# Kernel optimization log

Measured on AMD Instinct MI355X. Metric: run time of the kernel, lower is better.

## Reference

```python
import jax, jax.numpy as jnp
import numpy as np

B, L, D_MODEL = 2, 4096, 512
HEADS = 8
DH = D_MODEL // HEADS
M = 266  # round(DH * ln(DH)) = round(64 * 4.1589)


def setup_inputs() -> dict:
    key = jax.random.key(0)
    ks = jax.random.split(key, 12)
    s = 0.02
    d = D_MODEL
    return {
        "query": jax.random.normal(ks[0], (B, L, d), jnp.float32),
        "key": jax.random.normal(ks[1], (B, L, d), jnp.float32),
        "value": jax.random.normal(ks[2], (B, L, d), jnp.float32),
        "Wq": jax.random.normal(ks[3], (d, d), jnp.float32) * s,
        "bq": jnp.zeros((d,), jnp.float32),
        "Wk": jax.random.normal(ks[4], (d, d), jnp.float32) * s,
        "bk": jnp.zeros((d,), jnp.float32),
        "Wv": jax.random.normal(ks[5], (d, d), jnp.float32) * s,
        "bv": jnp.zeros((d,), jnp.float32),
        "Wout": jax.random.normal(ks[6], (d, d), jnp.float32) * s,
        "bout": jnp.zeros((d,), jnp.float32),
        "random_features": jax.random.normal(ks[7], (M, DH), jnp.float32),
    }


def reference(query, key, value, Wq, bq, Wk, bk, Wv, bv, Wout, bout, random_features):
    bs, sl, dm = query.shape
    H, Dh = HEADS, dm // HEADS

    def lin(x, W, b):
        return x @ W.T + b

    def to_heads(x):  # [B,L,dm] -> [L,B,H,Dh]  (matches torch [L,B,H,*] layout)
        return x.reshape(bs, sl, H, Dh).transpose(1, 0, 2, 3)

    q = to_heads(lin(query, Wq, bq))
    k = to_heads(lin(key, Wk, bk))
    v = to_heads(lin(value, Wv, bv))

    scale = dm ** 0.25
    q = q / scale
    k = k / scale

    # project onto random features: W_t is random_features^T, [Dh,M]
    pq = jnp.einsum('lbhd,md->lbhm', q, random_features)
    pk = jnp.einsum('lbhd,md->lbhm', k, random_features)
    # exp kernel: exp(h + x) with h = -||x||^2 / 2
    hq = -0.5 * jnp.sum(q * q, axis=-1, keepdims=True)
    hk = -0.5 * jnp.sum(k * k, axis=-1, keepdims=True)
    q_prime = jnp.exp(hq + pq)  # [L,B,H,M]
    k_prime = jnp.exp(hk + pk)  # [L,B,H,M]

    # Causal FAVOR+ numerator/denominator via prefix-sum recurrence (lax.scan over L)
    def step(carry, xs):
        S, z = carry           # S: [B,H,M,Dh], z: [B,H,M]
        qt, kt, vt = xs        # [B,H,M], [B,H,M], [B,H,Dh]
        S = S + kt[..., None] * vt[..., None, :]
        z = z + kt
        num = jnp.einsum('bhmd,bhm->bhd', S, qt)
        den = jnp.einsum('bhm,bhm->bh', qt, z)
        return (S, z), (num, den)

    S0 = jnp.zeros((bs, H, M, Dh), q.dtype)
    z0 = jnp.zeros((bs, H, M), q.dtype)
    _, (num, den) = jax.lax.scan(step, (S0, z0), (q_prime, k_prime, v))

    attn = num / den[..., None]                     # [L,B,H,Dh]
    ctx = attn.transpose(1, 0, 2, 3).reshape(bs, sl, dm)
    return ctx @ Wout.T + bout
```

## Files before the change

kernel.cpp:

```cpp
#include <hip/hip_runtime.h>
#include <hip/hip_bf16.h>

#define L_ 4096
#define MP 272
#define BH16 16

typedef __attribute__((ext_vector_type(8))) __bf16 bf16x8;
typedef __attribute__((ext_vector_type(4))) float f32x4;

__device__ inline __bf16 f2b(float f) {
    unsigned u = __float_as_uint(f);
    unsigned r = (u + 0x7fffu + ((u >> 16) & 1u)) >> 16;
    unsigned short s = (unsigned short)r;
    return *reinterpret_cast<__bf16*>(&s);
}
__device__ inline float b2f(__bf16 b) {
    unsigned short s = *reinterpret_cast<unsigned short*>(&b);
    return __uint_as_float(((unsigned)s) << 16);
}

#define NW 262144
__global__ __launch_bounds__(256) void prep2(
    const float* __restrict__ Wq, const float* __restrict__ Wk, const float* __restrict__ Wv,
    const float* __restrict__ Wout, const float* __restrict__ RF,
    __bf16* __restrict__ Wqb, __bf16* __restrict__ Wkb, __bf16* __restrict__ Wvb,
    __bf16* __restrict__ Woutb, __bf16* __restrict__ RFb, __bf16* __restrict__ vT)
{
    long idx = (long)blockIdx.x * 256 + threadIdx.x;
    if (idx < NW) { Wqb[idx] = f2b(Wq[idx]); return; }  idx -= NW;
    if (idx < NW) { Wkb[idx] = f2b(Wk[idx]); return; }  idx -= NW;
    if (idx < NW) { Wvb[idx] = f2b(Wv[idx]); return; }  idx -= NW;
    if (idx < NW) { Woutb[idx] = f2b(Wout[idx]); return; }  idx -= NW;
    if (idx < MP * 64) { int row = (int)(idx >> 6); RFb[idx] = f2b(row < 266 ? RF[idx] : 0.f); return; }
    idx -= MP * 64;
    if (idx < 65536) {
        int bh = (int)(idx >> 12), l = (int)(idx & 4095);
        vT[((size_t)bh * 65 + 64) * L_ + l] = f2b(1.f);
    }
}

template<int AF32, int EPI>
__global__ __launch_bounds__(512) void proj(
    const void* __restrict__ Ap, const __bf16* __restrict__ W,
    const float* __restrict__ bias, void* __restrict__ O,
    float* __restrict__ hout, float scale)
{
    __shared__ __bf16 Al[128 * 40];
    __shared__ __bf16 Bl[64 * 40];
    const int t = threadIdx.x;
    const int w = t >> 6, lane = t & 63;
    const int m0 = blockIdx.x * 128, n0 = blockIdx.y * 64;

    f32x4 acc[4];
    #pragma unroll
    for (int j = 0; j < 4; ++j) acc[j] = f32x4{0.f,0.f,0.f,0.f};

    float4 a_f[2];
    unsigned a_h[4];
    unsigned b_r[2];

    auto LOADT = [&](int ks) {
        const int kk = ks * 32;
        if constexpr (AF32) {
            const float* A = (const float*)Ap;
            #pragma unroll
            for (int it = 0; it < 2; ++it) {
                int u = t + it * 512; int r = u >> 3, q4 = (u & 7) << 2;
                a_f[it] = *(const float4*)&A[(size_t)(m0 + r) * 512 + kk + q4];
            }
        } else {
            const __bf16* A = (const __bf16*)Ap;
            #pragma unroll
            for (int it = 0; it < 4; ++it) {
                int u = t + it * 512; int r = u >> 4, dw = (u & 15) << 1;
                a_h[it] = *(const unsigned*)&A[(size_t)(m0 + r) * 512 + kk + dw];
            }
        }
        #pragma unroll
        for (int it = 0; it < 2; ++it) {
            int u = t + it * 512; int r = u >> 4, dw = (u & 15) << 1;
            b_r[it] = *(const unsigned*)&W[(size_t)(n0 + r) * 512 + kk + dw];
        }
    };
    auto STORET = [&]() {
        if constexpr (AF32) {
            #pragma unroll
            for (int it = 0; it < 2; ++it) {
                int u = t + it * 512; int r = u >> 3, q4 = (u & 7) << 2;
                __bf16* d = &Al[r * 40 + q4];
                d[0] = f2b(a_f[it].x); d[1] = f2b(a_f[it].y);
                d[2] = f2b(a_f[it].z); d[3] = f2b(a_f[it].w);
            }
        } else {
            #pragma unroll
            for (int it = 0; it < 4; ++it) {
                int u = t + it * 512; int r = u >> 4, dw = (u & 15) << 1;
                *(unsigned*)&Al[r * 40 + dw] = a_h[it];
            }
        }
        #pragma unroll
        for (int it = 0; it < 2; ++it) {
            int u = t + it * 512; int r = u >> 4, dw = (u & 15) << 1;
            *(unsigned*)&Bl[r * 40 + dw] = b_r[it];
        }
    };

    LOADT(0);
    for (int ks = 0; ks < 16; ++ks) {
        __syncthreads();
        STORET();
        __syncthreads();
        if (ks < 15) LOADT(ks + 1);
        bf16x8 af = *(const bf16x8*)&Al[(w * 16 + (lane & 15)) * 40 + (lane >> 4) * 8];
        #pragma unroll
        for (int j = 0; j < 4; ++j) {
            bf16x8 bf = *(const bf16x8*)&Bl[(j * 16 + (lane & 15)) * 40 + (lane >> 4) * 8];
            acc[j] = __builtin_amdgcn_mfma_f32_16x16x32_bf16(af, bf, acc[j], 0, 0, 0);
        }
    }

    if constexpr (EPI == 1) {
        __shared__ __bf16 Tv[64 * 136];
        #pragma unroll
        for (int j = 0; j < 4; ++j)
            #pragma unroll
            for (int e = 0; e < 4; ++e) {
                int rl = w * 16 + ((lane >> 4) << 2) + e;
                int cn = n0 + j * 16 + (lane & 15);
                Tv[(cn & 63) * 136 + rl] = f2b(acc[j][e] + bias[cn]);
            }
        __syncthreads();
        __bf16* vT = (__bf16*)O;
        int b = m0 >> 12, l0 = m0 & 4095, h = n0 >> 6;
        #pragma unroll
        for (int it = 0; it < 2; ++it) {
            int v = t + it * 512;
            int d = v >> 4, seg = v & 15;
            *(uint4*)&vT[((size_t)(b * 8 + h) * 65 + d) * L_ + l0 + seg * 8] =
                *(const uint4*)&Tv[d * 136 + seg * 8];
        }
    } else if constexpr (EPI == 0) {
        float sred[4] = {0.f, 0.f, 0.f, 0.f};
        #pragma unroll
        for (int j = 0; j < 4; ++j)
            #pragma unroll
            for (int e = 0; e < 4; ++e) {
                int r = m0 + w * 16 + ((lane >> 4) << 2) + e;
                int cn = n0 + j * 16 + (lane & 15);
                float vv = (acc[j][e] + bias[cn]) * scale;
                int b = r >> 12, l = r & 4095, h = cn >> 6, d = cn & 63;
                ((__bf16*)O)[(((size_t)(b * 8 + h) * L_ + l) << 6) + d] = f2b(vv);
                sred[e] += vv * vv;
            }
        #pragma unroll
        for (int e = 0; e < 4; ++e) {
            float s = sred[e];
            s += __shfl_xor(s, 1); s += __shfl_xor(s, 2);
            s += __shfl_xor(s, 4); s += __shfl_xor(s, 8);
            if ((lane & 15) == 0) {
                int r = m0 + w * 16 + ((lane >> 4) << 2) + e;
                int bh = (r >> 12) * 8 + (n0 >> 6);
                hout[(size_t)bh * 4096 + (r & 4095)] = -0.5f * s;
            }
        }
    } else {
        #pragma unroll
        for (int j = 0; j < 4; ++j)
            #pragma unroll
            for (int e = 0; e < 4; ++e) {
                int r = m0 + w * 16 + ((lane >> 4) << 2) + e;
                int cn = n0 + j * 16 + (lane & 15);
                ((float*)O)[(size_t)r * 512 + cn] = acc[j][e] + bias[cn];
            }
    }
}

__global__ __launch_bounds__(256) void chunk_sums4(
    const __bf16* __restrict__ kh, const __bf16* __restrict__ vT,
    const float* __restrict__ hk, const __bf16* __restrict__ RFb,
    __bf16* __restrict__ ScT)
{
    __shared__ char arena[41472];
    __bf16* RFl = (__bf16*)(arena);
    __bf16* KPl = (__bf16*)(arena + 9216);
    __bf16* Vl  = (__bf16*)(arena + 18432);
    __bf16* T2  = (__bf16*)(arena + 29952);
    const int t = threadIdx.x;
    const int w = t >> 6, lane = t & 63;
    const int z = blockIdx.x, zb = z & 15, zc = z >> 4;
    const __bf16* kh_b = kh + (size_t)zb * 262144 + (size_t)(zc * 64) * 64;
    const __bf16* vT_b = vT + (size_t)zb * 266240 + (size_t)zc * 64;
    __bf16* Obase = ScT + (size_t)(zc * 16 + zb) * 17680;

    bf16x8 ak[2];
    #pragma unroll
    for (int ks = 0; ks < 2; ++ks)
        ak[ks] = *(const bf16x8*)&kh_b[(size_t)(w * 16 + (lane & 15)) * 64 + ks * 32 + (lane >> 4) * 8];
    float hkr[4];
    #pragma unroll
    for (int e = 0; e < 4; ++e)
        hkr[e] = hk[(size_t)zb * 4096 + zc * 64 + w * 16 + ((lane >> 4) << 2) + e];

    #pragma unroll
    for (int it = 0; it < 9; ++it) {
        int u = t + it * 256;
        if (u < 2080) {
            int d = u >> 5, lp = (u & 31) << 1;
            *(unsigned*)&Vl[d * 72 + lp] = *(const unsigned*)&vT_b[(size_t)d * L_ + lp];
        }
    }

    for (int mt = 0; mt < 5; ++mt) {
        const int m0 = mt * 64;
        __syncthreads();
        #pragma unroll
        for (int it = 0; it < 8; ++it) {
            int u = t + it * 256; int r = u >> 5, lp = (u & 31) << 1;
            unsigned v = (m0 + r < MP) ? *(const unsigned*)&RFb[(size_t)(m0 + r) * 64 + lp] : 0u;
            *(unsigned*)&RFl[r * 72 + lp] = v;
        }
        __syncthreads();
        f32x4 acck[4];
        #pragma unroll
        for (int j = 0; j < 4; ++j) acck[j] = f32x4{0.f,0.f,0.f,0.f};
        #pragma unroll
        for (int ks = 0; ks < 2; ++ks)
            #pragma unroll
            for (int j = 0; j < 4; ++j) {
                bf16x8 bf = *(const bf16x8*)&RFl[(j * 16 + (lane & 15)) * 72 + ks * 32 + (lane >> 4) * 8];
                acck[j] = __builtin_amdgcn_mfma_f32_16x16x32_bf16(ak[ks], bf, acck[j], 0, 0, 0);
            }
        #pragma unroll
        for (int j = 0; j < 4; ++j)
            #pragma unroll
            for (int e = 0; e < 4; ++e) {
                int rl = w * 16 + ((lane >> 4) << 2) + e;
                int cn = j * 16 + (lane & 15);
                float v = (m0 + cn < 266) ? __expf(hkr[e] + acck[j][e]) : 0.f;
                KPl[cn * 72 + rl] = f2b(v);
            }
        __syncthreads();
        f32x4 accS[5];
        #pragma unroll
        for (int j = 0; j < 5; ++j) accS[j] = f32x4{0.f,0.f,0.f,0.f};
        #pragma unroll
        for (int ks = 0; ks < 2; ++ks) {
            bf16x8 af = *(const bf16x8*)&KPl[(w * 16 + (lane & 15)) * 72 + ks * 32 + (lane >> 4) * 8];
            #pragma unroll
            for (int j = 0; j < 5; ++j) {
                bf16x8 bf = *(const bf16x8*)&Vl[(j * 16 + (lane & 15)) * 72 + ks * 32 + (lane >> 4) * 8];
                accS[j] = __builtin_amdgcn_mfma_f32_16x16x32_bf16(af, bf, accS[j], 0, 0, 0);
            }
        }
        #pragma unroll
        for (int j = 0; j < 5; ++j)
            #pragma unroll
            for (int e = 0; e < 4; ++e) {
                int rl = w * 16 + ((lane >> 4) << 2) + e;
                int cn = j * 16 + (lane & 15);
                T2[cn * 72 + rl] = f2b(accS[j][e]);
            }
        __syncthreads();
        for (int v2 = t; v2 < 65 * 8; v2 += 256) {
            int row = v2 >> 3, seg = v2 & 7;
            if (m0 + seg * 8 < MP)
                *(uint4*)&Obase[(size_t)row * MP + m0 + seg * 8] = *(const uint4*)&T2[row * 72 + seg * 8];
        }
    }
}

__global__ __launch_bounds__(256) void prefixk(__bf16* __restrict__ ScT)
{
    int idx = blockIdx.x * 256 + threadIdx.x;
    const int STRIDE = BH16 * 65 * MP;
    if (idx >= STRIDE) return;
    __bf16* p = ScT + idx;
    float run = 0.f;
    #pragma unroll 1
    for (int cb = 0; cb < 8; ++cb) {
        float v[8];
        #pragma unroll
        for (int i = 0; i < 8; ++i) v[i] = b2f(p[(size_t)(cb * 8 + i) * STRIDE]);
        #pragma unroll
        for (int i = 0; i < 8; ++i) { p[(size_t)(cb * 8 + i) * STRIDE] = f2b(run); run += v[i]; }
    }
}

__global__ __launch_bounds__(256) void fusedD2(
    const __bf16* __restrict__ qh, const __bf16* __restrict__ kh,
    const float* __restrict__ hq, const float* __restrict__ hk,
    const __bf16* __restrict__ RFb, const __bf16* __restrict__ ScT,
    const __bf16* __restrict__ vT, __bf16* __restrict__ ctx)
{
    __shared__ char arena[41728];
    __bf16* RFl = (__bf16*)(arena);
    __bf16* Vl  = (__bf16*)(arena);
    __bf16* B2l = (__bf16*)(arena + 11520);
    __bf16* Aq  = (__bf16*)(arena + 23040);
    __bf16* Bk  = (__bf16*)(arena + 32256);
    __bf16* Sl  = (__bf16*)(arena + 32256);
    float* sden = (float*)(arena + 41472);
    const int t = threadIdx.x;
    const int w = t >> 6, lane = t & 63;
    const int z = blockIdx.x, zb = z & 15, zc = z >> 4;
    const __bf16* qh_b = qh + (size_t)zb * 262144 + (size_t)(zc * 64) * 64;
    const __bf16* kh_b = kh + (size_t)zb * 262144 + (size_t)(zc * 64) * 64;
    const __bf16* Sp_b = ScT + (size_t)(zc * 16 + zb) * 17680;
    const __bf16* vT_b = vT + (size_t)zb * 266240 + (size_t)zc * 64;

    bf16x8 aq[2], ak[2];
    #pragma unroll
    for (int ks = 0; ks < 2; ++ks) {
        size_t off = (size_t)(w * 16 + (lane & 15)) * 64 + ks * 32 + (lane >> 4) * 8;
        aq[ks] = *(const bf16x8*)&qh_b[off];
        ak[ks] = *(const bf16x8*)&kh_b[off];
    }
    float hqr[4], hkr[4];
    #pragma unroll
    for (int e = 0; e < 4; ++e) {
        int rl = w * 16 + ((lane >> 4) << 2) + e;
        hqr[e] = hq[(size_t)zb * 4096 + zc * 64 + rl];
        hkr[e] = hk[(size_t)zb * 4096 + zc * 64 + rl];
    }
    unsigned v_r[10];
    #pragma unroll
    for (int it = 0; it < 10; ++it) {
        int u = t + it * 256; int d = u >> 5, lp = (u & 31) << 1;
        v_r[it] = (d < 65) ? *(const unsigned*)&vT_b[(size_t)d * L_ + lp] : 0u;
    }

    f32x4 acc1[4], acc2[5];
    #pragma unroll
    for (int j = 0; j < 4; ++j) acc1[j] = f32x4{0.f,0.f,0.f,0.f};
    #pragma unroll
    for (int j = 0; j < 5; ++j) acc2[j] = f32x4{0.f,0.f,0.f,0.f};

    for (int mt = 0; mt < 5; ++mt) {
        const int m0 = mt * 64;
        __syncthreads();
        #pragma unroll
        for (int it = 0; it < 8; ++it) {
            int u = t + it * 256; int r = u >> 5, lp = (u & 31) << 1;
            unsigned v = (m0 + r < MP) ? *(const unsigned*)&RFb[(size_t)(m0 + r) * 64 + lp] : 0u;
            *(unsigned*)&RFl[r * 72 + lp] = v;
        }
        #pragma unroll
        for (int it = 0; it < 9; ++it) {
            int u = t + it * 256;
            if (u < 2080) {
                int r = u >> 5, lp = (u & 31) << 1;
                unsigned v = (m0 + lp < MP) ? *(const unsigned*)&Sp_b[(size_t)r * MP + m0 + lp] : 0u;
                *(unsigned*)&B2l[r * 72 + lp] = v;
            }
        }
        __syncthreads();
        f32x4 accq[4], acck[4];
        #pragma unroll
        for (int j = 0; j < 4; ++j) { accq[j] = f32x4{0.f,0.f,0.f,0.f}; acck[j] = f32x4{0.f,0.f,0.f,0.f}; }
        #pragma unroll
        for (int ks = 0; ks < 2; ++ks)
            #pragma unroll
            for (int j = 0; j < 4; ++j) {
                bf16x8 bf = *(const bf16x8*)&RFl[(j * 16 + (lane & 15)) * 72 + ks * 32 + (lane >> 4) * 8];
                accq[j] = __builtin_amdgcn_mfma_f32_16x16x32_bf16(aq[ks], bf, accq[j], 0, 0, 0);
                acck[j] = __builtin_amdgcn_mfma_f32_16x16x32_bf16(ak[ks], bf, acck[j], 0, 0, 0);
            }
        #pragma unroll
        for (int j = 0; j < 4; ++j)
            #pragma unroll
            for (int e = 0; e < 4; ++e) {
                int rl = w * 16 + ((lane >> 4) << 2) + e;
                int cn = j * 16 + (lane & 15);
                bool ok = (m0 + cn) < 266;
                Aq[rl * 72 + cn] = f2b(ok ? __expf(hqr[e] + accq[j][e]) : 0.f);
                Bk[rl * 72 + cn] = f2b(ok ? __expf(hkr[e] + acck[j][e]) : 0.f);
            }
        __syncthreads();
        #pragma unroll
        for (int ks = 0; ks < 2; ++ks) {
            bf16x8 af = *(const bf16x8*)&Aq[(w * 16 + (lane & 15)) * 72 + ks * 32 + (lane >> 4) * 8];
            #pragma unroll
            for (int j = 0; j < 4; ++j) {
                bf16x8 bf = *(const bf16x8*)&Bk[(j * 16 + (lane & 15)) * 72 + ks * 32 + (lane >> 4) * 8];
                acc1[j] = __builtin_amdgcn_mfma_f32_16x16x32_bf16(af, bf, acc1[j], 0, 0, 0);
            }
            #pragma unroll
            for (int j = 0; j < 5; ++j) {
                bf16x8 bf = *(const bf16x8*)&B2l[(j * 16 + (lane & 15)) * 72 + ks * 32 + (lane >> 4) * 8];
                acc2[j] = __builtin_amdgcn_mfma_f32_16x16x32_bf16(af, bf, acc2[j], 0, 0, 0);
            }
        }
    }
    __syncthreads();
    #pragma unroll
    for (int it = 0; it < 10; ++it) {
        int u = t + it * 256; int d = u >> 5, lp = (u & 31) << 1;
        *(unsigned*)&Vl[d * 72 + lp] = v_r[it];
    }
    #pragma unroll
    for (int j = 0; j < 4; ++j)
        #pragma unroll
        for (int e = 0; e < 4; ++e) {
            int rl = w * 16 + ((lane >> 4) << 2) + e;
            int cn = j * 16 + (lane & 15);
            Sl[rl * 72 + cn] = f2b(rl >= cn ? acc1[j][e] : 0.f);
        }
    __syncthreads();
    #pragma unroll
    for (int ks2 = 0; ks2 < 2; ++ks2) {
        bf16x8 as = *(const bf16x8*)&Sl[(w * 16 + (lane & 15)) * 72 + ks2 * 32 + (lane >> 4) * 8];
        #pragma unroll
        for (int j = 0; j < 5; ++j) {
            bf16x8 bf = *(const bf16x8*)&Vl[(j * 16 + (lane & 15)) * 72 + ks2 * 32 + (lane >> 4) * 8];
            acc2[j] = __builtin_amdgcn_mfma_f32_16x16x32_bf16(as, bf, acc2[j], 0, 0, 0);
        }
    }
    if ((lane & 15) == 0) {
        #pragma unroll
        for (int e = 0; e < 4; ++e)
            sden[w * 16 + ((lane >> 4) << 2) + e] = acc2[4][e];
    }
    __syncthreads();
    const int b = zb >> 3, h = zb & 7;
    #pragma unroll
    for (int j = 0; j < 4; ++j)
        #pragma unroll
        for (int e = 0; e < 4; ++e) {
            int rl = w * 16 + ((lane >> 4) << 2) + e;
            int cn = j * 16 + (lane & 15);
            float val = acc2[j][e] / sden[rl];
            ctx[((size_t)(b * L_ + zc * 64 + rl)) * 512 + h * 64 + cn] = f2b(val);
        }
}

extern "C" void kernel_launch(void* const* d_in, const int* in_sizes, int n_in,
                              void* d_out, int out_size, void* d_ws, size_t ws_size,
                              hipStream_t stream) {
    const float* query = (const float*)d_in[0];
    const float* key   = (const float*)d_in[1];
    const float* value = (const float*)d_in[2];
    const float* Wq    = (const float*)d_in[3];
    const float* bq    = (const float*)d_in[4];
    const float* Wk    = (const float*)d_in[5];
    const float* bk    = (const float*)d_in[6];
    const float* Wv    = (const float*)d_in[7];
    const float* bv    = (const float*)d_in[8];
    const float* Wout  = (const float*)d_in[9];
    const float* bout  = (const float*)d_in[10];
    const float* RF    = (const float*)d_in[11];

    char* w8 = (char*)d_ws;
    __bf16* ctx  = (__bf16*)(w8 + 0);
    __bf16* qh   = (__bf16*)(w8 + 8388608);
    __bf16* kh   = (__bf16*)(w8 + 16777216);
    __bf16* vT   = (__bf16*)(w8 + 25165824);
    __bf16* ScT  = (__bf16*)(w8 + 33688576);
    __bf16* Wqb  = (__bf16*)(w8 + 69897216);
    __bf16* Wkb  = (__bf16*)(w8 + 70421504);
    __bf16* Wvb  = (__bf16*)(w8 + 70945792);
    __bf16* Woutb= (__bf16*)(w8 + 71470080);
    __bf16* RFb  = (__bf16*)(w8 + 71994368);
    float*  hq   = (float*) (w8 + 72029184);
    float*  hk   = (float*) (w8 + 72291328);

    const float qscale = 0.21022410381342865f;

    prep2<<<4420, 256, 0, stream>>>(Wq, Wk, Wv, Wout, RF, Wqb, Wkb, Wvb, Woutb, RFb, vT);

    dim3 gg(64, 8);
    proj<1,0><<<gg, 512, 0, stream>>>(query, Wqb, bq, qh, hq, qscale);
    proj<1,0><<<gg, 512, 0, stream>>>(key,   Wkb, bk, kh, hk, qscale);
    proj<1,1><<<gg, 512, 0, stream>>>(value, Wvb, bv, vT, nullptr, 1.f);

    chunk_sums4<<<1024, 256, 0, stream>>>(kh, vT, hk, RFb, ScT);

    prefixk<<<1105, 256, 0, stream>>>(ScT);

    fusedD2<<<1024, 256, 0, stream>>>(qh, kh, hq, hk, RFb, ScT, vT, ctx);

    proj<0,2><<<gg, 512, 0, stream>>>(ctx, Woutb, bout, d_out, nullptr, 1.f);
}
```

Baseline: 276.2 us.

## Register-prefetch next RF/prefix tiles and drop intra-tile barriers in FAVOR kernels

In both the chunk-sum kernel and the fused output kernel, the next m-tile of random features (and, in the fused kernel, the prefix-state tile) is loaded into registers while the current tile is computed. It is written to LDS at the end of the iteration, which leaves one barrier per tile instead of two. The chunk-sum kernel also swaps MFMA operand roles so that each wave owns the feature rows it writes, which removes the barrier between the exp step and the S accumulation. The fused kernel issues the Aq×S MFMAs before the barrier, because those rows are wave-private. The cost is higher register pressure, which could reduce occupancy.

```diff
diff --git a/kernel.cpp b/kernel.cpp
--- a/kernel.cpp
+++ b/kernel.cpp
@@ -175,12 +175,12 @@
     }
 }
 
-__global__ __launch_bounds__(256) void chunk_sums4(
+__global__ __launch_bounds__(256) void chunk_sums6(
     const __bf16* __restrict__ kh, const __bf16* __restrict__ vT,
     const float* __restrict__ hk, const __bf16* __restrict__ RFb,
     __bf16* __restrict__ ScT)
 {
-    __shared__ char arena[41472];
+    __shared__ char arena[39456];
     __bf16* RFl = (__bf16*)(arena);
     __bf16* KPl = (__bf16*)(arena + 9216);
     __bf16* Vl  = (__bf16*)(arena + 18432);
@@ -192,54 +192,66 @@
     const __bf16* vT_b = vT + (size_t)zb * 266240 + (size_t)zc * 64;
     __bf16* Obase = ScT + (size_t)(zc * 16 + zb) * 17680;
 
-    bf16x8 ak[2];
-    #pragma unroll
-    for (int ks = 0; ks < 2; ++ks)
-        ak[ks] = *(const bf16x8*)&kh_b[(size_t)(w * 16 + (lane & 15)) * 64 + ks * 32 + (lane >> 4) * 8];
-    float hkr[4];
-    #pragma unroll
-    for (int e = 0; e < 4; ++e)
-        hkr[e] = hk[(size_t)zb * 4096 + zc * 64 + w * 16 + ((lane >> 4) << 2) + e];
-
-    #pragma unroll
-    for (int it = 0; it < 9; ++it) {
-        int u = t + it * 256;
-        if (u < 2080) {
-            int d = u >> 5, lp = (u & 31) << 1;
-            *(unsigned*)&Vl[d * 72 + lp] = *(const unsigned*)&vT_b[(size_t)d * L_ + lp];
-        }
-    }
+    bf16x8 bkh[4][2];
+    #pragma unroll
+    for (int j = 0; j < 4; ++j)
+        #pragma unroll
+        for (int ks = 0; ks < 2; ++ks)
+            bkh[j][ks] = *(const bf16x8*)&kh_b[(size_t)(j * 16 + (lane & 15)) * 64 + ks * 32 + (lane >> 4) * 8];
+    float hk_c[4];
+    #pragma unroll
+    for (int j = 0; j < 4; ++j)
+        hk_c[j] = hk[(size_t)zb * 4096 + zc * 64 + j * 16 + (lane & 15)];
+
+    unsigned rf_r[8];
+    auto LOAD_RF = [&](int mt) {
+        const int m0 = mt * 64;
+        #pragma unroll
+        for (int it = 0; it < 8; ++it) {
+            int u = t + it * 256; int r = u >> 5, lp = (u & 31) << 1;
+            rf_r[it] = (m0 + r < MP) ? *(const unsigned*)&RFb[(size_t)(m0 + r) * 64 + lp] : 0u;
+        }
+    };
+    auto STAGE_RF = [&]() {
+        #pragma unroll
+        for (int it = 0; it < 8; ++it) {
+            int u = t + it * 256; int r = u >> 5, lp = (u & 31) << 1;
+            *(unsigned*)&RFl[r * 72 + lp] = rf_r[it];
+        }
+    };
+
+    #pragma unroll
+    for (int it = 0; it < 10; ++it) {
+        int u = t + it * 256; int d = u >> 5, lp = (u & 31) << 1;
+        unsigned v = (d < 65) ? *(const unsigned*)&vT_b[(size_t)d * L_ + lp] : 0u;
+        *(unsigned*)&Vl[d * 72 + lp] = v;
+    }
+    LOAD_RF(0);
+    STAGE_RF();
+    __syncthreads();
 
     for (int mt = 0; mt < 5; ++mt) {
         const int m0 = mt * 64;
-        __syncthreads();
-        #pragma unroll
-        for (int it = 0; it < 8; ++it) {
-            int u = t + it * 256; int r = u >> 5, lp = (u & 31) << 1;
-            unsigned v = (m0 + r < MP) ? *(const unsigned*)&RFb[(size_t)(m0 + r) * 64 + lp] : 0u;
-            *(unsigned*)&RFl[r * 72 + lp] = v;
-        }
-        __syncthreads();
+        if (mt < 4) LOAD_RF(mt + 1);
         f32x4 acck[4];
         #pragma unroll
         for (int j = 0; j < 4; ++j) acck[j] = f32x4{0.f,0.f,0.f,0.f};
         #pragma unroll
-        for (int ks = 0; ks < 2; ++ks)
-            #pragma unroll
-            for (int j = 0; j < 4; ++j) {
-                bf16x8 bf = *(const bf16x8*)&RFl[(j * 16 + (lane & 15)) * 72 + ks * 32 + (lane >> 4) * 8];
-                acck[j] = __builtin_amdgcn_mfma_f32_16x16x32_bf16(ak[ks], bf, acck[j], 0, 0, 0);
-            }
+        for (int ks = 0; ks < 2; ++ks) {
+            bf16x8 af = *(const bf16x8*)&RFl[(w * 16 + (lane & 15)) * 72 + ks * 32 + (lane >> 4) * 8];
+            #pragma unroll
+            for (int j = 0; j < 4; ++j)
+                acck[j] = __builtin_amdgcn_mfma_f32_16x16x32_bf16(af, bkh[j][ks], acck[j], 0, 0, 0);
+        }
         #pragma unroll
         for (int j = 0; j < 4; ++j)
             #pragma unroll
             for (int e = 0; e < 4; ++e) {
                 int rl = w * 16 + ((lane >> 4) << 2) + e;
                 int cn = j * 16 + (lane & 15);
-                float v = (m0 + cn < 266) ? __expf(hkr[e] + acck[j][e]) : 0.f;
-                KPl[cn * 72 + rl] = f2b(v);
-            }
-        __syncthreads();
+                float v = (m0 + rl < 266) ? __expf(hk_c[j] + acck[j][e]) : 0.f;
+                KPl[rl * 72 + cn] = f2b(v);
+            }
         f32x4 accS[5];
         #pragma unroll
         for (int j = 0; j < 5; ++j) accS[j] = f32x4{0.f,0.f,0.f,0.f};
@@ -258,7 +270,7 @@
             for (int e = 0; e < 4; ++e) {
                 int rl = w * 16 + ((lane >> 4) << 2) + e;
                 int cn = j * 16 + (lane & 15);
-                T2[cn * 72 + rl] = f2b(accS[j][e]);
+                if (cn < 66) T2[cn * 72 + rl] = f2b(accS[j][e]);
             }
         __syncthreads();
         for (int v2 = t; v2 < 65 * 8; v2 += 256) {
@@ -266,6 +278,8 @@
             if (m0 + seg * 8 < MP)
                 *(uint4*)&Obase[(size_t)row * MP + m0 + seg * 8] = *(const uint4*)&T2[row * 72 + seg * 8];
         }
+        if (mt < 4) STAGE_RF();
+        __syncthreads();
     }
 }
 
@@ -286,20 +300,20 @@
     }
 }
 
-__global__ __launch_bounds__(256) void fusedD2(
+__global__ __launch_bounds__(256) void fusedD3(
     const __bf16* __restrict__ qh, const __bf16* __restrict__ kh,
     const float* __restrict__ hq, const float* __restrict__ hk,
     const __bf16* __restrict__ RFb, const __bf16* __restrict__ ScT,
     const __bf16* __restrict__ vT, __bf16* __restrict__ ctx)
 {
-    __shared__ char arena[41728];
+    __shared__ char arena[39424];
     __bf16* RFl = (__bf16*)(arena);
+    __bf16* B2l = (__bf16*)(arena + 9216);
     __bf16* Vl  = (__bf16*)(arena);
-    __bf16* B2l = (__bf16*)(arena + 11520);
-    __bf16* Aq  = (__bf16*)(arena + 23040);
-    __bf16* Bk  = (__bf16*)(arena + 32256);
-    __bf16* Sl  = (__bf16*)(arena + 32256);
-    float* sden = (float*)(arena + 41472);
+    __bf16* Aq  = (__bf16*)(arena + 20736);
+    __bf16* Bk  = (__bf16*)(arena + 29952);
+    __bf16* Sl  = (__bf16*)(arena + 29952);
+    float* sden = (float*)(arena + 39168);
     const int t = threadIdx.x;
     const int w = t >> 6, lane = t & 63;
     const int z = blockIdx.x, zb = z & 15, zc = z >> 4;
@@ -308,12 +322,12 @@
     const __bf16* Sp_b = ScT + (size_t)(zc * 16 + zb) * 17680;
     const __bf16* vT_b = vT + (size_t)zb * 266240 + (size_t)zc * 64;
 
-    bf16x8 aq[2], ak[2];
+    bf16x8 aq[2], akk[2];
     #pragma unroll
     for (int ks = 0; ks < 2; ++ks) {
         size_t off = (size_t)(w * 16 + (lane & 15)) * 64 + ks * 32 + (lane >> 4) * 8;
         aq[ks] = *(const bf16x8*)&qh_b[off];
-        ak[ks] = *(const bf16x8*)&kh_b[off];
+        akk[ks] = *(const bf16x8*)&kh_b[off];
     }
     float hqr[4], hkr[4];
     #pragma unroll
@@ -329,31 +343,46 @@
         v_r[it] = (d < 65) ? *(const unsigned*)&vT_b[(size_t)d * L_ + lp] : 0u;
     }
 
+    unsigned rf_r[8], sp_r[10];
+    auto LOAD = [&](int mt) {
+        const int m0 = mt * 64;
+        #pragma unroll
+        for (int it = 0; it < 8; ++it) {
+            int u = t + it * 256; int r = u >> 5, lp = (u & 31) << 1;
+            rf_r[it] = (m0 + r < MP) ? *(const unsigned*)&RFb[(size_t)(m0 + r) * 64 + lp] : 0u;
+        }
+        #pragma unroll
+        for (int it = 0; it < 10; ++it) {
+            int u = t + it * 256; int r = u >> 5, lp = (u & 31) << 1;
+            sp_r[it] = (r < 65 && m0 + lp < MP) ? *(const unsigned*)&Sp_b[(size_t)r * MP + m0 + lp] : 0u;
+        }
+    };
+    auto STAGE = [&]() {
+        #pragma unroll
+        for (int it = 0; it < 8; ++it) {
+            int u = t + it * 256; int r = u >> 5, lp = (u & 31) << 1;
+            *(unsigned*)&RFl[r * 72 + lp] = rf_r[it];
+        }
+        #pragma unroll
+        for (int it = 0; it < 10; ++it) {
+            int u = t + it * 256; int r = u >> 5, lp = (u & 31) << 1;
+            *(unsigned*)&B2l[r * 72 + lp] = sp_r[it];
+        }
+    };
+
     f32x4 acc1[4], acc2[5];
     #pragma unroll
     for (int j = 0; j < 4; ++j) acc1[j] = f32x4{0.f,0.f,0.f,0.f};
     #pragma unroll
     for (int j = 0; j < 5; ++j) acc2[j] = f32x4{0.f,0.f,0.f,0.f};
+
+    LOAD(0);
+    STAGE();
+    __syncthreads();
 
     for (int mt = 0; mt < 5; ++mt) {
         const int m0 = mt * 64;
-        __syncthreads();
-        #pragma unroll
-        for (int it = 0; it < 8; ++it) {
-            int u = t + it * 256; int r = u >> 5, lp = (u & 31) << 1;
-            unsigned v = (m0 + r < MP) ? *(const unsigned*)&RFb[(size_t)(m0 + r) * 64 + lp] : 0u;
-            *(unsigned*)&RFl[r * 72 + lp] = v;
-        }
-        #pragma unroll
-        for (int it = 0; it < 9; ++it) {
-            int u = t + it * 256;
-            if (u < 2080) {
-                int r = u >> 5, lp = (u & 31) << 1;
-                unsigned v = (m0 + lp < MP) ? *(const unsigned*)&Sp_b[(size_t)r * MP + m0 + lp] : 0u;
-                *(unsigned*)&B2l[r * 72 + lp] = v;
-            }
-        }
-        __syncthreads();
+        if (mt < 4) LOAD(mt + 1);
         f32x4 accq[4], acck[4];
         #pragma unroll
         for (int j = 0; j < 4; ++j) { accq[j] = f32x4{0.f,0.f,0.f,0.f}; acck[j] = f32x4{0.f,0.f,0.f,0.f}; }
@@ -363,7 +392,7 @@
             for (int j = 0; j < 4; ++j) {
                 bf16x8 bf = *(const bf16x8*)&RFl[(j * 16 + (lane & 15)) * 72 + ks * 32 + (lane >> 4) * 8];
                 accq[j] = __builtin_amdgcn_mfma_f32_16x16x32_bf16(aq[ks], bf, accq[j], 0, 0, 0);
-                acck[j] = __builtin_amdgcn_mfma_f32_16x16x32_bf16(ak[ks], bf, acck[j], 0, 0, 0);
+                acck[j] = __builtin_amdgcn_mfma_f32_16x16x32_bf16(akk[ks], bf, acck[j], 0, 0, 0);
             }
         #pragma unroll
         for (int j = 0; j < 4; ++j)
@@ -375,23 +404,29 @@
                 Aq[rl * 72 + cn] = f2b(ok ? __expf(hqr[e] + accq[j][e]) : 0.f);
                 Bk[rl * 72 + cn] = f2b(ok ? __expf(hkr[e] + acck[j][e]) : 0.f);
             }
-        __syncthreads();
-        #pragma unroll
-        for (int ks = 0; ks < 2; ++ks) {
-            bf16x8 af = *(const bf16x8*)&Aq[(w * 16 + (lane & 15)) * 72 + ks * 32 + (lane >> 4) * 8];
+        bf16x8 af[2];
+        #pragma unroll
+        for (int ks = 0; ks < 2; ++ks)
+            af[ks] = *(const bf16x8*)&Aq[(w * 16 + (lane & 15)) * 72 + ks * 32 + (lane >> 4) * 8];
+        #pragma unroll
+        for (int ks = 0; ks < 2; ++ks)
+            #pragma unroll
+            for (int j = 0; j < 5; ++j) {
+                bf16x8 bf = *(const bf16x8*)&B2l[(j * 16 + (lane & 15)) * 72 + ks * 32 + (lane >> 4) * 8];
+                acc2[j] = __builtin_amdgcn_mfma_f32_16x16x32_bf16(af[ks], bf, acc2[j], 0, 0, 0);
+            }
+        __syncthreads();
+        #pragma unroll
+        for (int ks = 0; ks < 2; ++ks)
             #pragma unroll
             for (int j = 0; j < 4; ++j) {
                 bf16x8 bf = *(const bf16x8*)&Bk[(j * 16 + (lane & 15)) * 72 + ks * 32 + (lane >> 4) * 8];
-                acc1[j] = __builtin_amdgcn_mfma_f32_16x16x32_bf16(af, bf, acc1[j], 0, 0, 0);
-            }
-            #pragma unroll
-            for (int j = 0; j < 5; ++j) {
-                bf16x8 bf = *(const bf16x8*)&B2l[(j * 16 + (lane & 15)) * 72 + ks * 32 + (lane >> 4) * 8];
-                acc2[j] = __builtin_amdgcn_mfma_f32_16x16x32_bf16(af, bf, acc2[j], 0, 0, 0);
-            }
-        }
-    }
-    __syncthreads();
+                acc1[j] = __builtin_amdgcn_mfma_f32_16x16x32_bf16(af[ks], bf, acc1[j], 0, 0, 0);
+            }
+        if (mt < 4) STAGE();
+        __syncthreads();
+    }
+
     #pragma unroll
     for (int it = 0; it < 10; ++it) {
         int u = t + it * 256; int d = u >> 5, lp = (u & 31) << 1;
@@ -472,11 +507,11 @@
     proj<1,0><<<gg, 512, 0, stream>>>(key,   Wkb, bk, kh, hk, qscale);
     proj<1,1><<<gg, 512, 0, stream>>>(value, Wvb, bv, vT, nullptr, 1.f);
 
-    chunk_sums4<<<1024, 256, 0, stream>>>(kh, vT, hk, RFb, ScT);
+    chunk_sums6<<<1024, 256, 0, stream>>>(kh, vT, hk, RFb, ScT);
 
     prefixk<<<1105, 256, 0, stream>>>(ScT);
 
-    fusedD2<<<1024, 256, 0, stream>>>(qh, kh, hq, hk, RFb, ScT, vT, ctx);
+    fusedD3<<<1024, 256, 0, stream>>>(qh, kh, hq, hk, RFb, ScT, vT, ctx);
 
     proj<0,2><<<gg, 512, 0, stream>>>(ctx, Woutb, bout, d_out, nullptr, 1.f);
 }
```

New measurement: 229.9 us. -16.8%, faster.
